# Optimization experiments

Measured on AMD Instinct MI355X. Metric: run time of the kernel, lower is better.

Reference implementation:

```python
import itertools
import jax, jax.numpy as jnp
import numpy as np

B, S, D = 256, 49, 448          # batch, tokens (7x7), channels
H, KD, ED = 8, 32, 128          # heads, key_dim, expanded_key_dim (attn_ratio*key_dim)
QKV_OUT = H * (KD + KD + ED)    # 1536
MLP_HID = 4 * D                 # 1792
EPS = 1e-12
SCALE = KD ** -0.5


def _bias_idxs(resolution=7):
    points = list(itertools.product(range(resolution), range(resolution)))
    offsets, idxs = {}, []
    for p1 in points:
        for p2 in points:
            off = (abs(p1[0] - p2[0]), abs(p1[1] - p2[1]))
            if off not in offsets:
                offsets[off] = len(offsets)
            idxs.append(offsets[off])
    n = len(points)
    return np.asarray(idxs, np.int32).reshape(n, n), len(offsets)


def setup_inputs() -> dict:
    key = jax.random.key(0)
    ks = jax.random.split(key, 12)
    idxs_np, n_off = _bias_idxs(7)  # [49,49], 49 offsets
    s = 0.02
    return {
        "hidden_states": jax.random.normal(ks[0], (B, S, D), jnp.float32),
        "ln2_w": jnp.ones((D,), jnp.float32),
        "ln2_b": jnp.zeros((D,), jnp.float32),
        "qkv_w": jax.random.normal(ks[1], (QKV_OUT, D), jnp.float32) * s,
        "qkv_b": jnp.zeros((QKV_OUT,), jnp.float32),
        "proj_w": jax.random.normal(ks[2], (D, H * ED), jnp.float32) * s,
        "proj_b": jnp.zeros((D,), jnp.float32),
        "attention_biases": jax.random.normal(ks[3], (H, n_off), jnp.float32) * s,
        "fc1_w": jax.random.normal(ks[4], (MLP_HID, D), jnp.float32) * s,
        "fc1_b": jnp.zeros((MLP_HID,), jnp.float32),
        "fc2_w": jax.random.normal(ks[5], (D, MLP_HID), jnp.float32) * s,
        "fc2_b": jnp.zeros((D,), jnp.float32),
        "layer_scale_1": jnp.full((D,), 1e-5, jnp.float32),
        "layer_scale_2": jnp.full((D,), 1e-5, jnp.float32),
        "attention_bias_idxs": jnp.asarray(idxs_np),  # int32 [49,49]
    }


def _layernorm(x, w, b):
    mu = jnp.mean(x, axis=-1, keepdims=True)
    var = jnp.mean(jnp.square(x - mu), axis=-1, keepdims=True)
    return (x - mu) * jax.lax.rsqrt(var + EPS) * w + b


def reference(hidden_states, ln2_w, ln2_b, qkv_w, qkv_b, proj_w, proj_b,
              attention_biases, fc1_w, fc1_b, fc2_w, fc2_b,
              layer_scale_1, layer_scale_2, attention_bias_idxs):
    # NOTE: upstream code applies norm2 before BOTH attention and MLP (faithful).
    norm = _layernorm(hidden_states, ln2_w, ln2_b)  # [B,S,D]

    qkv = (norm @ qkv_w.T + qkv_b).reshape(B, S, H, KD + KD + ED)
    q, k, v = jnp.split(qkv, [KD, 2 * KD], axis=-1)  # [B,S,H,KD/KD/ED]

    bias = attention_biases[:, attention_bias_idxs]  # [H,S,S] gathered rel-pos bias
    scores = jnp.einsum("bqhd,bkhd->bhqk", q, k) * SCALE + bias[None]
    probs = jax.nn.softmax(scores, axis=-1)          # [B,H,S,S]

    ctx = jnp.einsum("bhqk,bkhd->bqhd", probs, v).reshape(B, S, H * ED)
    attn_out = ctx @ proj_w.T + proj_b               # [B,S,D]

    out = hidden_states + layer_scale_1 * attn_out
    mlp = jax.nn.gelu(norm @ fc1_w.T + fc1_b, approximate=False) @ fc2_w.T + fc2_b
    out = out + layer_scale_2 * mlp
    return out
```

## Files before the change

### kernel.cpp

```cpp
#include <hip/hip_runtime.h>
#include <hip/hip_bf16.h>
#include <cstdint>

#define B_    256
#define S_    49
#define D_    448
#define H_    8
#define NTOK  (B_*S_)
#define QKVO  1536
#define MLPH  1792
#define SCALE_ 0.17677669529663687f

using bf16x8  = __attribute__((ext_vector_type(8))) __bf16;
using ushort8 = __attribute__((ext_vector_type(8))) unsigned short;
using f32x4   = __attribute__((ext_vector_type(4))) float;

__device__ __forceinline__ unsigned short f2bf(float f){
  uint32_t u = __builtin_bit_cast(uint32_t, f);
  u += 0x7fffu + ((u >> 16) & 1u);
  return (unsigned short)(u >> 16);
}
__device__ __forceinline__ float b2f(unsigned short b){
  uint32_t u = ((uint32_t)b) << 16;
  return __builtin_bit_cast(float, u);
}

__device__ __forceinline__ void gload_lds16(const void* g, void* l){
  __builtin_amdgcn_global_load_lds(
      (const __attribute__((address_space(1))) void*)g,
      (__attribute__((address_space(3))) void*)l, 16, 0, 0);
}

#define P_S0 688128L
#define P_S1 1490944L
#define P_S2 1949696L
#define P_S3 2752512L
#define P_S4 2932736L
#define P_S5 2936064L
#define P_S6 2936576L
#define P_S7 2969344L
__global__ __launch_bounds__(256)
void prep_k(const float* __restrict__ qkvw, const float* __restrict__ fc1w,
            const float* __restrict__ projw, const float* __restrict__ fc2w,
            const float* __restrict__ ls1, const float* __restrict__ ls2,
            const float* __restrict__ qkvb, const float* __restrict__ fc1b,
            const float* __restrict__ projb, const float* __restrict__ fc2b,
            const float* __restrict__ attb, const int* __restrict__ idxs,
            unsigned short* __restrict__ wcat, unsigned short* __restrict__ wfused,
            float* __restrict__ cbig, float* __restrict__ cbv,
            float* __restrict__ biasf){
  const long i = (long)blockIdx.x * 256 + threadIdx.x;
  if (i < P_S0){
    wcat[i] = f2bf(qkvw[i]);
  } else if (i < P_S1){
    long j = i - P_S0;
    wcat[i] = f2bf(fc1w[j]);
  } else if (i < P_S2){
    long j = i - P_S1;
    long r = j / 1024, c = j - r*1024;
    wfused[r*2816 + c] = f2bf(projw[j]*ls1[r]);
  } else if (i < P_S3){
    long j = i - P_S2;
    long r = j / 1792, c = j - r*1792;
    wfused[r*2816 + 1024 + c] = f2bf(fc2w[j]*ls2[r]);
  } else if (i < P_S4){
    long j = i - P_S3;
    wfused[448L*2816 + j] = 0;
  } else if (i < P_S5){
    long j = i - P_S4;
    cbig[j] = (j < 1536) ? qkvb[j] : fc1b[j - 1536];
  } else if (i < P_S6){
    long j = i - P_S5;
    cbv[j] = (j < 448) ? ls1[j]*projb[j] + ls2[j]*fc2b[j] : 0.f;
  } else if (i < P_S7){
    long j = i - P_S6;
    int h = (int)(j >> 12), r = (int)((j >> 6) & 63), c = (int)(j & 63);
    float v;
    if (c >= 49) v = -1e30f;
    else { int q = r < 49 ? r : 48; v = attb[h*49 + idxs[q*49 + c]]; }
    biasf[j] = v;
  }
}

__global__ __launch_bounds__(448)
void ln_k(const float* __restrict__ x, const float* __restrict__ w,
          const float* __restrict__ b, unsigned short* __restrict__ out){
  const int tok = blockIdx.x, t = threadIdx.x;
  const float v = x[(size_t)tok*448 + t];
  float s1 = v, s2 = v*v;
  #pragma unroll
  for (int o = 32; o; o >>= 1){ s1 += __shfl_xor(s1, o); s2 += __shfl_xor(s2, o); }
  __shared__ float a1[7], a2[7];
  const int wid = t >> 6;
  if ((t & 63) == 0){ a1[wid] = s1; a2[wid] = s2; }
  __syncthreads();
  float S1 = 0.f, S2 = 0.f;
  #pragma unroll
  for (int i = 0; i < 7; ++i){ S1 += a1[i]; S2 += a2[i]; }
  const float mu  = S1 * (1.f/448.f);
  const float var = S2 * (1.f/448.f) - mu*mu;
  const float rs  = rsqrtf(var + 1e-12f);
  out[(size_t)tok*448 + t] = f2bf((v - mu)*rs*w[t] + b[t]);
}

template<int EPI>
__global__ __launch_bounds__(256)
void gemm_k(const unsigned short* __restrict__ A1, int lda1, int nkt1,
            const unsigned short* __restrict__ A2, int lda2, int nkt,
            const unsigned short* __restrict__ W, int ldw,
            const float* __restrict__ bias,
            const float* __restrict__ resid, float* __restrict__ outF,
            unsigned short* __restrict__ outB1, int ldo1,
            unsigned short* __restrict__ outB2, int ldo2,
            int splitBy, int nby)
{
  constexpr int BN = (EPI == 4) ? 128 : 64;
  constexpr int NF = BN/32;
  constexpr int SMEM = (EPI == 4) ? 65536 : 49152;
  __shared__ char smem[SMEM];

  const int NB = gridDim.x;
  const int q8 = NB >> 3, r8 = NB & 7;
  const int xcd = blockIdx.x & 7, idx = blockIdx.x >> 3;
  const int wgid = (xcd < r8 ? xcd*(q8+1) : r8*(q8+1) + (xcd-r8)*q8) + idx;
  const int bx = wgid / nby, by = wgid - bx*nby;

  const int t = threadIdx.x, lane = t & 63, wid = t >> 6;
  const int wm = wid >> 1, wn = wid & 1;
  const int g = lane >> 4, li = lane & 15;
  f32x4 acc[4][NF] = {};

  const int srow  = lane >> 3;
  const int scolw = ((lane & 7) ^ srow) * 8;

  auto stage = [&](int buf, int kt){
    char* Asb = smem + buf*16384;
    char* Bsb = smem + 32768 + buf*(BN*128);
    const unsigned short* Ab; int lda, k0;
    if (kt < nkt1){ Ab = A1; lda = lda1; k0 = kt*64; }
    else          { Ab = A2; lda = lda2; k0 = (kt - nkt1)*64; }
    #pragma unroll
    for (int i = 0; i < 4; ++i){
      const int c = wid*4 + i;
      gload_lds16(Ab + (size_t)(bx*128 + c*8 + srow)*lda + k0 + scolw,
                  Asb + c*1024);
    }
    #pragma unroll
    for (int i = 0; i < NF; ++i){
      const int c = wid*NF + i;
      gload_lds16(W + (size_t)(by*BN + c*8 + srow)*ldw + kt*64 + scolw,
                  Bsb + c*1024);
    }
  };

  int buf = 0;
  stage(0, 0);
  for (int kt = 0; kt < nkt; ++kt){
    __syncthreads();
    if (kt + 1 < nkt) stage(buf ^ 1, kt + 1);
    char* Asb = smem + buf*16384;
    char* Bsb = smem + 32768 + buf*(BN*128);
    #pragma unroll
    for (int ks = 0; ks < 2; ++ks){
      const int kk2 = (ks*32 + g*8)*2;
      bf16x8 af[4], bfr[NF];
      #pragma unroll
      for (int mf = 0; mf < 4; ++mf){
        const int row = wm*64 + mf*16 + li;
        af[mf] = *reinterpret_cast<const bf16x8*>(
            Asb + row*128 + (kk2 ^ ((row & 7) << 4)));
      }
      #pragma unroll
      for (int nf = 0; nf < NF; ++nf){
        const int row = wn*(BN/2) + nf*16 + li;
        bfr[nf] = *reinterpret_cast<const bf16x8*>(
            Bsb + row*128 + (kk2 ^ ((row & 7) << 4)));
      }
      #pragma unroll
      for (int mf = 0; mf < 4; ++mf)
        #pragma unroll
        for (int nf = 0; nf < NF; ++nf)
          acc[mf][nf] = __builtin_amdgcn_mfma_f32_16x16x32_bf16(af[mf], bfr[nf], acc[mf][nf], 0, 0, 0);
    }
    buf ^= 1;
  }
  __syncthreads();

  const int lr = lane >> 4, lc = lane & 15;
  if (EPI == 4){
    const bool dogelu = by >= splitBy;
    #pragma unroll
    for (int mf = 0; mf < 4; ++mf){
      #pragma unroll
      for (int nf = 0; nf < NF; ++nf){
        const int col = wn*64 + nf*16 + li;
        const float bi = bias[by*128 + col];
        #pragma unroll
        for (int j = 0; j < 4; ++j){
          const int row = wm*64 + mf*16 + g*4 + j;
          float v = acc[mf][nf][j] + bi;
          if (dogelu) v = 0.5f*v*(1.0f + erff(v*0.70710678118654752f));
          *reinterpret_cast<float*>(smem + row*512 + ((col*4) ^ (((row >> 2) & 3) << 6))) = v;
        }
      }
    }
    __syncthreads();
    #pragma unroll
    for (int it = 0; it < 8; ++it){
      const int r = wid*32 + it*4 + lr;
      const int sw = ((r >> 2) & 3) << 6;
      const f32x4 v0 = *reinterpret_cast<const f32x4*>(smem + r*512 + ((lc*32)      ^ sw));
      const f32x4 v1 = *reinterpret_cast<const f32x4*>(smem + r*512 + ((lc*32 + 16) ^ sw));
      ushort8 u;
      #pragma unroll
      for (int k = 0; k < 4; ++k){ u[k] = f2bf(v0[k]); u[4+k] = f2bf(v1[k]); }
      const int grow = bx*128 + r;
      if (by < splitBy)
        *reinterpret_cast<ushort8*>(outB1 + (size_t)grow*ldo1 + by*128 + lc*8) = u;
      else
        *reinterpret_cast<ushort8*>(outB2 + (size_t)grow*ldo2 + (by - splitBy)*128 + lc*8) = u;
    }
  } else {
    #pragma unroll
    for (int mf = 0; mf < 4; ++mf){
      #pragma unroll
      for (int nf = 0; nf < NF; ++nf){
        const int col = wn*32 + nf*16 + li;
        const float bi = bias[by*64 + col];
        #pragma unroll
        for (int j = 0; j < 4; ++j){
          const int rt = wm*64 + mf*16 + g*4 + j;
          *reinterpret_cast<float*>(smem + rt*256 + ((col*4) ^ (((rt >> 2) & 1) << 6)))
              = acc[mf][nf][j] + bi;
        }
      }
    }
    __syncthreads();
    #pragma unroll
    for (int i = 0; i < 8; ++i){
      const int r = wid*32 + i*4 + lr;
      const int sw = ((r >> 2) & 1) << 6;
      const f32x4 v = *reinterpret_cast<const f32x4*>(smem + r*256 + ((lc*16) ^ sw));
      const size_t o = (size_t)(bx*128 + r)*448 + by*64 + lc*4;
      const f32x4 rs = *reinterpret_cast<const f32x4*>(resid + o);
      *reinterpret_cast<f32x4*>(outF + o) = rs + v;
    }
  }
}

__global__ __launch_bounds__(256)
void attn_mfma_k(const unsigned short* __restrict__ qkv,
                 const float* __restrict__ biasf,
                 unsigned short* __restrict__ ctx)
{
  const int bh = blockIdx.x;
  const int b = bh >> 3, h = bh & 7;
  __shared__ unsigned short Vs[64*128];
  __shared__ unsigned short Ps[64*64];
  const int t = threadIdx.x, lane = t & 63, w = t >> 6;
  const int g = lane >> 4, li = lane & 15;
  const size_t qbase = ((size_t)b*49)*QKVO + (size_t)h*192;

  for (int c = t; c < 64*16; c += 256){
    const int k = c >> 4, seg = c & 15;
    bf16x8 v = {};
    if (k < 49)
      v = *reinterpret_cast<const bf16x8*>(qkv + qbase + 64 + (size_t)k*QKVO + seg*8);
    const int byte = (k*256 + seg*16) ^ ((((unsigned)k >> 3) & 3) << 5);
    *reinterpret_cast<bf16x8*>((char*)Vs + byte) = v;
  }

  const int qrow = w*16 + li;
  bf16x8 afq = {};
  if (qrow < 49)
    afq = *reinterpret_cast<const bf16x8*>(qkv + qbase + (size_t)qrow*QKVO + g*8);
  f32x4 accs[4];
  #pragma unroll
  for (int nf = 0; nf < 4; ++nf){
    const int krow = nf*16 + li;
    bf16x8 bfr = {};
    if (krow < 49)
      bfr = *reinterpret_cast<const bf16x8*>(qkv + qbase + 32 + (size_t)krow*QKVO + g*8);
    f32x4 z = {};
    accs[nf] = __builtin_amdgcn_mfma_f32_16x16x32_bf16(afq, bfr, z, 0, 0, 0);
  }

  #pragma unroll
  for (int j = 0; j < 4; ++j){
    const int row = w*16 + g*4 + j;
    float sv[4];
    #pragma unroll
    for (int nf = 0; nf < 4; ++nf)
      sv[nf] = accs[nf][j]*SCALE_ + biasf[h*4096 + row*64 + nf*16 + li];
    float m = fmaxf(fmaxf(sv[0], sv[1]), fmaxf(sv[2], sv[3]));
    #pragma unroll
    for (int o = 8; o; o >>= 1) m = fmaxf(m, __shfl_xor(m, o));
    float e[4], s = 0.f;
    #pragma unroll
    for (int nf = 0; nf < 4; ++nf){ e[nf] = __expf(sv[nf] - m); s += e[nf]; }
    #pragma unroll
    for (int o = 8; o; o >>= 1) s += __shfl_xor(s, o);
    const float inv = 1.f / s;
    #pragma unroll
    for (int nf = 0; nf < 4; ++nf){
      const int byte = (row*128 + (nf*16 + li)*2) ^ ((row & 7) << 4);
      *reinterpret_cast<unsigned short*>((char*)Ps + byte) = f2bf(e[nf]*inv);
    }
  }
  __syncthreads();

  f32x4 accp[4][2] = {};
  #pragma unroll
  for (int kt = 0; kt < 2; ++kt){
    bf16x8 pa[4];
    #pragma unroll
    for (int mt = 0; mt < 4; ++mt){
      const int q = mt*16 + li;
      const int byte = (q*128 + kt*64 + g*16) ^ ((q & 7) << 4);
      pa[mt] = *reinterpret_cast<const bf16x8*>((char*)Ps + byte);
    }
    #pragma unroll
    for (int nf = 0; nf < 2; ++nf){
      const int d = w*32 + nf*16 + li;
      ushort8 vbu;
      #pragma unroll
      for (int j = 0; j < 8; ++j){
        const int k = kt*32 + g*8 + j;
        const int byte = (k*256 + d*2) ^ ((((unsigned)k >> 3) & 3) << 5);
        vbu[j] = *reinterpret_cast<const unsigned short*>((char*)Vs + byte);
      }
      const bf16x8 vb = __builtin_bit_cast(bf16x8, vbu);
      #pragma unroll
      for (int mt = 0; mt < 4; ++mt)
        accp[mt][nf] = __builtin_amdgcn_mfma_f32_16x16x32_bf16(pa[mt], vb, accp[mt][nf], 0, 0, 0);
    }
  }

  const size_t obase = ((size_t)b*49)*1024 + (size_t)h*128;
  #pragma unroll
  for (int mt = 0; mt < 4; ++mt){
    #pragma unroll
    for (int nf = 0; nf < 2; ++nf){
      #pragma unroll
      for (int j = 0; j < 4; ++j){
        const int row = mt*16 + g*4 + j;
        if (row < 49){
          const int col = w*32 + nf*16 + li;
          ctx[obase + (size_t)row*1024 + col] = f2bf(accp[mt][nf][j]);
        }
      }
    }
  }
}

extern "C" void kernel_launch(void* const* d_in, const int* in_sizes, int n_in,
                              void* d_out, int out_size, void* d_ws, size_t ws_size,
                              hipStream_t stream)
{
  const float* hidden = (const float*)d_in[0];
  const float* ln2w   = (const float*)d_in[1];
  const float* ln2b   = (const float*)d_in[2];
  const float* qkvw   = (const float*)d_in[3];
  const float* qkvb   = (const float*)d_in[4];
  const float* projw  = (const float*)d_in[5];
  const float* projb  = (const float*)d_in[6];
  const float* attb   = (const float*)d_in[7];
  const float* fc1w   = (const float*)d_in[8];
  const float* fc1b   = (const float*)d_in[9];
  const float* fc2w   = (const float*)d_in[10];
  const float* fc2b   = (const float*)d_in[11];
  const float* ls1    = (const float*)d_in[12];
  const float* ls2    = (const float*)d_in[13];
  const int*   aidx   = (const int*)d_in[14];
  float* out = (float*)d_out;

  char* p = (char*)d_ws;
  auto alloc = [&](size_t bytes){ void* r = (void*)p; p += (bytes + 255) & ~(size_t)255; return r; };
  unsigned short* wcat   = (unsigned short*)alloc((size_t)3328*448*2);
  unsigned short* wfused = (unsigned short*)alloc((size_t)512*2816*2);
  unsigned short* normb  = (unsigned short*)alloc((size_t)NTOK*448*2);
  unsigned short* qkvv   = (unsigned short*)alloc((size_t)NTOK*QKVO*2);
  unsigned short* ctx    = (unsigned short*)alloc((size_t)NTOK*1024*2);
  unsigned short* hid    = (unsigned short*)alloc((size_t)NTOK*MLPH*2);
  float*          biasf  = (float*)alloc((size_t)8*64*64*4);
  float*          cbig   = (float*)alloc((size_t)3328*4);
  float*          cbv    = (float*)alloc((size_t)512*4);

  prep_k<<<(int)(P_S7/256), 256, 0, stream>>>(qkvw, fc1w, projw, fc2w, ls1, ls2,
                                              qkvb, fc1b, projb, fc2b, attb, aidx,
                                              wcat, wfused, cbig, cbv, biasf);
  ln_k<<<NTOK, 448, 0, stream>>>(hidden, ln2w, ln2b, normb);

  gemm_k<4><<<98*26, 256, 0, stream>>>(normb, 448, 7, nullptr, 448, 7,
                                       wcat, 448, cbig,
                                       nullptr, nullptr,
                                       qkvv, QKVO, hid, MLPH, 12, 26);
  attn_mfma_k<<<B_*H_, 256, 0, stream>>>(qkvv, biasf, ctx);
  gemm_k<1><<<98*7, 256, 0, stream>>>(ctx, 1024, 16, hid, MLPH, 44,
                                      wfused, 2816, cbv,
                                      hidden, out,
                                      nullptr, 0, nullptr, 0, 999, 7);
}
```

Baseline: 163.6 us.

## Use 256x256 tiles with 512 threads for the QKV/FC1 GEMM

The first GEMM (norm x concatenated QKV+FC1 weights) moves from a templated 128x128 tile kernel with 256 threads to a dedicated kernel with 256x256 tiles, 8 waves and 128 KB of shared memory. Each wave now computes 128x64 of output. The epilogue is split into two halves that reuse the staging buffer. This raises reuse per loaded byte and cuts the block count from 2548 to 637. In exchange, shared-memory use and register pressure go up, occupancy drops, and tail or wave-quantisation effects may appear with fewer, larger blocks.

```diff
diff --git a/kernel.cpp b/kernel.cpp
--- a/kernel.cpp
+++ b/kernel.cpp
@@ -103,21 +103,126 @@
   out[(size_t)tok*448 + t] = f2bf((v - mu)*rs*w[t] + b[t]);
 }
 
-template<int EPI>
+__global__ __launch_bounds__(512, 2)
+void gemm4_k(const unsigned short* __restrict__ A,
+             const unsigned short* __restrict__ W,
+             const float* __restrict__ bias,
+             unsigned short* __restrict__ outB1,
+             unsigned short* __restrict__ outB2,
+             int splitBy, int nby)
+{
+  __shared__ char smem[131072];
+
+  const int NB = gridDim.x;
+  const int q8 = NB >> 3, r8 = NB & 7;
+  const int xcd = blockIdx.x & 7, idx = blockIdx.x >> 3;
+  const int wgid = (xcd < r8 ? xcd*(q8+1) : r8*(q8+1) + (xcd-r8)*q8) + idx;
+  const int bx = wgid / nby, by = wgid - bx*nby;
+
+  const int t = threadIdx.x, lane = t & 63, wid = t >> 6;
+  const int wm = wid >> 2, wn = wid & 3;
+  const int g = lane >> 4, li = lane & 15;
+  f32x4 acc[8][4] = {};
+
+  const int srow  = lane >> 3;
+  const int scolw = ((lane & 7) ^ srow) * 8;
+
+  auto stage = [&](int buf, int kt){
+    char* Asb = smem + buf*32768;
+    char* Bsb = smem + 65536 + buf*32768;
+    const int k0 = kt*64;
+    #pragma unroll
+    for (int i = 0; i < 4; ++i){
+      const int c = wid*4 + i;
+      gload_lds16(A + (size_t)(bx*256 + c*8 + srow)*448 + k0 + scolw, Asb + c*1024);
+      gload_lds16(W + (size_t)(by*256 + c*8 + srow)*448 + k0 + scolw, Bsb + c*1024);
+    }
+  };
+
+  int buf = 0;
+  stage(0, 0);
+  for (int kt = 0; kt < 7; ++kt){
+    __syncthreads();
+    if (kt + 1 < 7) stage(buf ^ 1, kt + 1);
+    char* Asb = smem + buf*32768;
+    char* Bsb = smem + 65536 + buf*32768;
+    #pragma unroll
+    for (int ks = 0; ks < 2; ++ks){
+      const int kk2 = (ks*32 + g*8)*2;
+      bf16x8 af[8], bfr[4];
+      #pragma unroll
+      for (int mf = 0; mf < 8; ++mf){
+        const int row = wm*128 + mf*16 + li;
+        af[mf] = *reinterpret_cast<const bf16x8*>(
+            Asb + row*128 + (kk2 ^ ((row & 7) << 4)));
+      }
+      #pragma unroll
+      for (int nf = 0; nf < 4; ++nf){
+        const int row = wn*64 + nf*16 + li;
+        bfr[nf] = *reinterpret_cast<const bf16x8*>(
+            Bsb + row*128 + (kk2 ^ ((row & 7) << 4)));
+      }
+      #pragma unroll
+      for (int mf = 0; mf < 8; ++mf)
+        #pragma unroll
+        for (int nf = 0; nf < 4; ++nf)
+          acc[mf][nf] = __builtin_amdgcn_mfma_f32_16x16x32_bf16(af[mf], bfr[nf], acc[mf][nf], 0, 0, 0);
+    }
+    buf ^= 1;
+  }
+  __syncthreads();
+
+  const bool dogelu = by >= splitBy;
+  const int lr = t >> 5, lc = t & 31;
+  #pragma unroll
+  for (int p = 0; p < 2; ++p){
+    if (p) __syncthreads();
+    if (wm == p){
+      #pragma unroll
+      for (int mf = 0; mf < 8; ++mf){
+        #pragma unroll
+        for (int nf = 0; nf < 4; ++nf){
+          const int col = wn*64 + nf*16 + li;
+          const float bi = bias[by*256 + col];
+          #pragma unroll
+          for (int j = 0; j < 4; ++j){
+            const int rt = mf*16 + g*4 + j;
+            float v = acc[mf][nf][j] + bi;
+            if (dogelu) v = 0.5f*v*(1.0f + erff(v*0.70710678118654752f));
+            *reinterpret_cast<float*>(smem + rt*1024 + ((col*4) ^ (((rt >> 2) & 3) << 6))) = v;
+          }
+        }
+      }
+    }
+    __syncthreads();
+    #pragma unroll
+    for (int it = 0; it < 8; ++it){
+      const int rt = it*16 + lr;
+      const int sw = ((rt >> 2) & 3) << 6;
+      const f32x4 v0 = *reinterpret_cast<const f32x4*>(smem + rt*1024 + ((lc*32)      ^ sw));
+      const f32x4 v1 = *reinterpret_cast<const f32x4*>(smem + rt*1024 + ((lc*32 + 16) ^ sw));
+      ushort8 u;
+      #pragma unroll
+      for (int k = 0; k < 4; ++k){ u[k] = f2bf(v0[k]); u[4+k] = f2bf(v1[k]); }
+      const int grow = bx*256 + p*128 + rt;
+      if (by < splitBy)
+        *reinterpret_cast<ushort8*>(outB1 + (size_t)grow*QKVO + by*256 + lc*8) = u;
+      else
+        *reinterpret_cast<ushort8*>(outB2 + (size_t)grow*MLPH + (by - splitBy)*256 + lc*8) = u;
+    }
+  }
+}
+
 __global__ __launch_bounds__(256)
-void gemm_k(const unsigned short* __restrict__ A1, int lda1, int nkt1,
-            const unsigned short* __restrict__ A2, int lda2, int nkt,
-            const unsigned short* __restrict__ W, int ldw,
-            const float* __restrict__ bias,
-            const float* __restrict__ resid, float* __restrict__ outF,
-            unsigned short* __restrict__ outB1, int ldo1,
-            unsigned short* __restrict__ outB2, int ldo2,
-            int splitBy, int nby)
+void gemm1_k(const unsigned short* __restrict__ A1, int lda1, int nkt1,
+             const unsigned short* __restrict__ A2, int lda2, int nkt,
+             const unsigned short* __restrict__ W, int ldw,
+             const float* __restrict__ bias,
+             const float* __restrict__ resid, float* __restrict__ outF,
+             int nby)
 {
-  constexpr int BN = (EPI == 4) ? 128 : 64;
-  constexpr int NF = BN/32;
-  constexpr int SMEM = (EPI == 4) ? 65536 : 49152;
-  __shared__ char smem[SMEM];
+  constexpr int BN = 64, NF = 2;
+  __shared__ char smem[49152];
 
   const int NB = gridDim.x;
   const int q8 = NB >> 3, r8 = NB & 7;
@@ -187,64 +292,29 @@
   __syncthreads();
 
   const int lr = lane >> 4, lc = lane & 15;
-  if (EPI == 4){
-    const bool dogelu = by >= splitBy;
-    #pragma unroll
-    for (int mf = 0; mf < 4; ++mf){
-      #pragma unroll
-      for (int nf = 0; nf < NF; ++nf){
-        const int col = wn*64 + nf*16 + li;
-        const float bi = bias[by*128 + col];
-        #pragma unroll
-        for (int j = 0; j < 4; ++j){
-          const int row = wm*64 + mf*16 + g*4 + j;
-          float v = acc[mf][nf][j] + bi;
-          if (dogelu) v = 0.5f*v*(1.0f + erff(v*0.70710678118654752f));
-          *reinterpret_cast<float*>(smem + row*512 + ((col*4) ^ (((row >> 2) & 3) << 6))) = v;
-        }
-      }
-    }
-    __syncthreads();
-    #pragma unroll
-    for (int it = 0; it < 8; ++it){
-      const int r = wid*32 + it*4 + lr;
-      const int sw = ((r >> 2) & 3) << 6;
-      const f32x4 v0 = *reinterpret_cast<const f32x4*>(smem + r*512 + ((lc*32)      ^ sw));
-      const f32x4 v1 = *reinterpret_cast<const f32x4*>(smem + r*512 + ((lc*32 + 16) ^ sw));
-      ushort8 u;
-      #pragma unroll
-      for (int k = 0; k < 4; ++k){ u[k] = f2bf(v0[k]); u[4+k] = f2bf(v1[k]); }
-      const int grow = bx*128 + r;
-      if (by < splitBy)
-        *reinterpret_cast<ushort8*>(outB1 + (size_t)grow*ldo1 + by*128 + lc*8) = u;
-      else
-        *reinterpret_cast<ushort8*>(outB2 + (size_t)grow*ldo2 + (by - splitBy)*128 + lc*8) = u;
-    }
-  } else {
-    #pragma unroll
-    for (int mf = 0; mf < 4; ++mf){
-      #pragma unroll
-      for (int nf = 0; nf < NF; ++nf){
-        const int col = wn*32 + nf*16 + li;
-        const float bi = bias[by*64 + col];
-        #pragma unroll
-        for (int j = 0; j < 4; ++j){
-          const int rt = wm*64 + mf*16 + g*4 + j;
-          *reinterpret_cast<float*>(smem + rt*256 + ((col*4) ^ (((rt >> 2) & 1) << 6)))
-              = acc[mf][nf][j] + bi;
-        }
-      }
-    }
-    __syncthreads();
-    #pragma unroll
-    for (int i = 0; i < 8; ++i){
-      const int r = wid*32 + i*4 + lr;
-      const int sw = ((r >> 2) & 1) << 6;
-      const f32x4 v = *reinterpret_cast<const f32x4*>(smem + r*256 + ((lc*16) ^ sw));
-      const size_t o = (size_t)(bx*128 + r)*448 + by*64 + lc*4;
-      const f32x4 rs = *reinterpret_cast<const f32x4*>(resid + o);
-      *reinterpret_cast<f32x4*>(outF + o) = rs + v;
-    }
+  #pragma unroll
+  for (int mf = 0; mf < 4; ++mf){
+    #pragma unroll
+    for (int nf = 0; nf < NF; ++nf){
+      const int col = wn*32 + nf*16 + li;
+      const float bi = bias[by*64 + col];
+      #pragma unroll
+      for (int j = 0; j < 4; ++j){
+        const int rt = wm*64 + mf*16 + g*4 + j;
+        *reinterpret_cast<float*>(smem + rt*256 + ((col*4) ^ (((rt >> 2) & 1) << 6)))
+            = acc[mf][nf][j] + bi;
+      }
+    }
+  }
+  __syncthreads();
+  #pragma unroll
+  for (int i = 0; i < 8; ++i){
+    const int r = wid*32 + i*4 + lr;
+    const int sw = ((r >> 2) & 1) << 6;
+    const f32x4 v = *reinterpret_cast<const f32x4*>(smem + r*256 + ((lc*16) ^ sw));
+    const size_t o = (size_t)(bx*128 + r)*448 + by*64 + lc*4;
+    const f32x4 rs = *reinterpret_cast<const f32x4*>(resid + o);
+    *reinterpret_cast<f32x4*>(outF + o) = rs + v;
   }
 }
 
@@ -391,13 +461,9 @@
                                               wcat, wfused, cbig, cbv, biasf);
   ln_k<<<NTOK, 448, 0, stream>>>(hidden, ln2w, ln2b, normb);
 
-  gemm_k<4><<<98*26, 256, 0, stream>>>(normb, 448, 7, nullptr, 448, 7,
-                                       wcat, 448, cbig,
-                                       nullptr, nullptr,
-                                       qkvv, QKVO, hid, MLPH, 12, 26);
+  gemm4_k<<<49*13, 512, 0, stream>>>(normb, wcat, cbig, qkvv, hid, 6, 13);
   attn_mfma_k<<<B_*H_, 256, 0, stream>>>(qkvv, biasf, ctx);
-  gemm_k<1><<<98*7, 256, 0, stream>>>(ctx, 1024, 16, hid, MLPH, 44,
-                                      wfused, 2816, cbv,
-                                      hidden, out,
-                                      nullptr, 0, nullptr, 0, 999, 7);
-}
+  gemm1_k<<<98*7, 256, 0, stream>>>(ctx, 1024, 16, hid, MLPH, 44,
+                                    wfused, 2816, cbv,
+                                    hidden, out, 7);
+}
```

New measurement: 195.9 us. +19.8%, slower.
